# Performance work log

Measured on AMD Instinct MI355X. Metric: run time of the kernel, lower is better.

## Reference

```python
import jax, jax.numpy as jnp
import numpy as np

N_NODES = 50000


def graph_conv(h, src, dst, W, b, num_nodes):
    """GCN-style conv: transform node features, then sum messages over edges.
    h: [N, Din], W: [Din, Dout] -> out: [N, Dout].
    """
    m = (h @ W)[src]                                   # [E, Dout] per-edge messages
    agg = jax.ops.segment_sum(m, dst, num_segments=num_nodes)  # [N, Dout]
    return agg + b


def setup_inputs() -> dict:
    key = jax.random.key(0)
    ks = jax.random.split(key, 8)
    N, E, D = N_NODES, 800000, 128
    s = 1.0 / np.sqrt(2 * D)
    return {
        "node_feature": jax.random.normal(ks[0], (N, D), jnp.float32),
        "H_prev": jax.random.normal(ks[1], (N, D), jnp.float32),
        "edge_index": jax.random.randint(ks[2], (2, E), 0, N, jnp.int32),
        "W_main": jax.random.normal(ks[3], (D, D), jnp.float32) / np.sqrt(D),
        "b_main": jnp.zeros((D,), jnp.float32),
        "W_z": jax.random.normal(ks[4], (2 * D, D), jnp.float32) * s,
        "b_z": jnp.zeros((D,), jnp.float32),
        "W_r": jax.random.normal(ks[5], (2 * D, D), jnp.float32) * s,
        "b_r": jnp.zeros((D,), jnp.float32),
        "W_h": jax.random.normal(ks[6], (2 * D, D), jnp.float32) * s,
        "b_h": jnp.zeros((D,), jnp.float32),
    }


def reference(node_feature, H_prev, edge_index, W_main, b_main,
              W_z, b_z, W_r, b_r, W_h, b_h):
    N = node_feature.shape[0]
    src, dst = edge_index[0], edge_index[1]
    # main message-passing layer + post-layer activation (ReLU)
    X = jax.nn.relu(graph_conv(node_feature, src, dst, W_main, b_main, N))
    # GRU-gated graph convolutions
    cat_zr = jnp.concatenate([X, H_prev], axis=1)       # [N, 2D]
    Z = jax.nn.sigmoid(graph_conv(cat_zr, src, dst, W_z, b_z, N))
    R = jax.nn.sigmoid(graph_conv(cat_zr, src, dst, W_r, b_r, N))
    cat_h = jnp.concatenate([X, R * H_prev], axis=1)
    H_tilde = jnp.tanh(graph_conv(cat_h, src, dst, W_h, b_h, N))
    H_out = Z * H_prev + (1.0 - Z) * H_tilde
    return H_out
```

## Files before the change

### kernel.cpp

```cpp
#include <hip/hip_runtime.h>
#include <hip/hip_fp16.h>
#include <math.h>

typedef _Float16 f16;
typedef f16 f16x2 __attribute__((ext_vector_type(2)));
typedef f16 f16x4 __attribute__((ext_vector_type(4)));
typedef f16 f16x8 __attribute__((ext_vector_type(8)));
typedef float f32x4_t __attribute__((ext_vector_type(4)));

__device__ __forceinline__ float sigmoidf(float x) {
  return 1.0f / (1.0f + __expf(-x));
}

#define GLDS16(gp, lp)                                                     \
  __builtin_amdgcn_global_load_lds(                                        \
      (const __attribute__((address_space(1))) void*)(gp),                 \
      (__attribute__((address_space(3))) void*)(lp), 16, 0, 0)

__global__ void zero_ints(int* __restrict__ p, int n) {
  int i = blockIdx.x * blockDim.x + threadIdx.x;
  if (i < n) p[i] = 0;
}

__global__ void bucket_hist(const int* __restrict__ dst, int* __restrict__ bcntP,
                            int E, int NB) {
  __shared__ int h[256];
  for (int i = threadIdx.x; i < NB; i += 256) h[i] = 0;
  __syncthreads();
  int base = (blockIdx.x * 256 + threadIdx.x) * 4;
  if (base + 3 < E) {
    int4 d = *(const int4*)&dst[base];
    atomicAdd(&h[d.x >> 8], 1);
    atomicAdd(&h[d.y >> 8], 1);
    atomicAdd(&h[d.z >> 8], 1);
    atomicAdd(&h[d.w >> 8], 1);
  } else {
    for (int e = base; e < E; ++e) atomicAdd(&h[dst[e] >> 8], 1);
  }
  __syncthreads();
  for (int i = threadIdx.x; i < NB; i += 256)
    if (h[i]) atomicAdd(&bcntP[i * 16], h[i]);
}

__global__ __launch_bounds__(256) void bucket_scan(const int* __restrict__ bcntP,
                                                   int* __restrict__ bbases,
                                                   int* __restrict__ gcurP, int NB) {
  __shared__ int wsum[4];
  const int tid = threadIdx.x, lane = tid & 63, wid = tid >> 6;
  int v = (tid < NB) ? bcntP[tid * 16] : 0;
  int x = v;
  #pragma unroll
  for (int d = 1; d < 64; d <<= 1) { int y = __shfl_up(x, d); if (lane >= d) x += y; }
  if (lane == 63) wsum[wid] = x;
  __syncthreads();
  if (wid == 0 && lane < 4) {
    int ws = wsum[lane];
    #pragma unroll
    for (int d = 1; d < 4; d <<= 1) { int y = __shfl_up(ws, d); if (lane >= d) ws += y; }
    wsum[lane] = ws;
  }
  __syncthreads();
  int excl = x - v + (wid ? wsum[wid - 1] : 0);
  if (tid < NB) { bbases[tid] = excl; gcurP[tid * 16] = excl; }
  if (tid == NB - 1) bbases[NB] = excl + v;
}

__global__ __launch_bounds__(256) void partition_v2(const int* __restrict__ src,
                                                    const int* __restrict__ dst,
                                                    int* __restrict__ gcurP,
                                                    unsigned int* __restrict__ bin,
                                                    int E, int NB) {
  __shared__ int bhist[256];
  __shared__ int bofs[257];
  __shared__ int gbase[256];
  __shared__ unsigned int recs[4096];
  const int tid = threadIdx.x;
  const int base = blockIdx.x * 4096;
  bhist[tid] = 0;
  __syncthreads();
  unsigned int rec[16];
  int bk[16];
  #pragma unroll
  for (int k = 0; k < 16; ++k) {
    int e = base + tid + k * 256;
    if (e < E) {
      int d = dst[e];
      rec[k] = (unsigned int)(src[e] & 0xFFFF) | ((unsigned int)(d & 255) << 16);
      bk[k] = d >> 8;
      atomicAdd(&bhist[bk[k]], 1);
    } else {
      bk[k] = -1;
    }
  }
  __syncthreads();
  if (tid < 64) {
    int l = tid;
    int v0 = bhist[4 * l], v1 = bhist[4 * l + 1];
    int v2 = bhist[4 * l + 2], v3 = bhist[4 * l + 3];
    int s1 = v0 + v1, s2 = s1 + v2, t = s2 + v3;
    int x = t;
    #pragma unroll
    for (int d = 1; d < 64; d <<= 1) { int y = __shfl_up(x, d); if (l >= d) x += y; }
    int basex = x - t;
    bofs[4 * l] = basex;
    bofs[4 * l + 1] = basex + v0;
    bofs[4 * l + 2] = basex + s1;
    bofs[4 * l + 3] = basex + s2;
    if (l == 63) bofs[256] = x;
  }
  __syncthreads();
  if (tid < NB && bhist[tid] > 0)
    gbase[tid] = atomicAdd(&gcurP[tid * 16], bhist[tid]);
  bhist[tid] = bofs[tid];
  __syncthreads();
  #pragma unroll
  for (int k = 0; k < 16; ++k) {
    if (bk[k] >= 0) {
      int p = atomicAdd(&bhist[bk[k]], 1);
      recs[p] = rec[k];
    }
  }
  __syncthreads();
  const int total = bofs[256];
  for (int i = tid; i < total; i += 256) {
    int lo = 0, hi = 256;
    #pragma unroll
    for (int s = 0; s < 8; ++s) {
      int mid = (lo + hi) >> 1;
      if (bofs[mid] <= i) lo = mid; else hi = mid;
    }
    bin[gbase[lo] + (i - bofs[lo])] = recs[i];
  }
}

__global__ __launch_bounds__(256) void bucket_sort(const unsigned int* __restrict__ bin,
                                                   const int* __restrict__ bbases,
                                                   unsigned short* __restrict__ eidx,
                                                   int* __restrict__ off,
                                                   int N, int NB) {
  const int b = blockIdx.x;
  const int bb = bbases[b], be = bbases[b + 1];
  const int cntb = be - bb;
  const int d0 = b << 8;
  const int ndst = min(256, N - d0);
  __shared__ int hist[256];
  __shared__ int lofs[256];
  __shared__ int cnt2[256];
  __shared__ unsigned short srt[8192];
  const int tid = threadIdx.x;
  hist[tid] = 0;
  cnt2[tid] = 0;
  __syncthreads();
  for (int i = bb + tid; i < be; i += 256)
    atomicAdd(&hist[(bin[i] >> 16) & 255], 1);
  __syncthreads();
  if (tid < 64) {
    int l = tid;
    int v0 = hist[4 * l], v1 = hist[4 * l + 1], v2 = hist[4 * l + 2], v3 = hist[4 * l + 3];
    int s1 = v0 + v1, s2 = s1 + v2, t = s2 + v3;
    int x = t;
    #pragma unroll
    for (int d = 1; d < 64; d <<= 1) { int y = __shfl_up(x, d); if (l >= d) x += y; }
    int basex = x - t;
    lofs[4 * l] = basex;
    lofs[4 * l + 1] = basex + v0;
    lofs[4 * l + 2] = basex + s1;
    lofs[4 * l + 3] = basex + s2;
  }
  __syncthreads();
  if (tid < ndst) off[d0 + tid] = bb + lofs[tid];
  if (b == NB - 1 && tid == 0) off[N] = be;
  if (cntb <= 8192) {
    for (int i = bb + tid; i < be; i += 256) {
      unsigned int r = bin[i];
      int ld = (r >> 16) & 255;
      int p = lofs[ld] + atomicAdd(&cnt2[ld], 1);
      srt[p] = (unsigned short)(r & 0xFFFF);
    }
    __syncthreads();
    for (int i = tid; i < cntb; i += 256) eidx[bb + i] = srt[i];
  } else {
    for (int i = bb + tid; i < be; i += 256) {
      unsigned int r = bin[i];
      int ld = (r >> 16) & 255;
      int p = bb + lofs[ld] + atomicAdd(&cnt2[ld], 1);
      eidx[p] = (unsigned short)(r & 0xFFFF);
    }
  }
}

__global__ void count_kernel(const int* __restrict__ dst, int* __restrict__ cnt, int E) {
  int base = (blockIdx.x * blockDim.x + threadIdx.x) * 4;
  if (base + 3 < E) {
    int4 d = *(const int4*)&dst[base];
    atomicAdd(&cnt[d.x], 1);
    atomicAdd(&cnt[d.y], 1);
    atomicAdd(&cnt[d.z], 1);
    atomicAdd(&cnt[d.w], 1);
  } else {
    for (int e = base; e < E; ++e) atomicAdd(&cnt[dst[e]], 1);
  }
}

__global__ __launch_bounds__(1024) void scan_local(const int* __restrict__ cnt,
                                                   int* __restrict__ off,
                                                   int* __restrict__ psum, int n) {
  __shared__ int wsum[16];
  const int tid = threadIdx.x, lane = tid & 63, wid = tid >> 6;
  int i = blockIdx.x * 1024 + tid;
  int v = (i < n) ? cnt[i] : 0;
  int x = v;
  #pragma unroll
  for (int d = 1; d < 64; d <<= 1) { int y = __shfl_up(x, d); if (lane >= d) x += y; }
  if (lane == 63) wsum[wid] = x;
  __syncthreads();
  if (wid == 0) {
    int ws = (lane < 16) ? wsum[lane] : 0;
    #pragma unroll
    for (int d = 1; d < 16; d <<= 1) { int y = __shfl_up(ws, d); if (lane >= d) ws += y; }
    if (lane < 16) wsum[lane] = ws;
  }
  __syncthreads();
  int excl = x - v + (wid ? wsum[wid - 1] : 0);
  if (i < n) off[i] = excl;
  if (tid == 1023) psum[blockIdx.x] = wsum[15];
}

__global__ __launch_bounds__(1024) void scan_carry(int* __restrict__ psum,
                                                   int* __restrict__ off,
                                                   int* __restrict__ cur, int nb, int n) {
  __shared__ int wsum[16];
  const int tid = threadIdx.x, lane = tid & 63, wid = tid >> 6;
  int v = (tid < nb) ? psum[tid] : 0;
  int x = v;
  #pragma unroll
  for (int d = 1; d < 64; d <<= 1) { int y = __shfl_up(x, d); if (lane >= d) x += y; }
  if (lane == 63) wsum[wid] = x;
  __syncthreads();
  if (wid == 0) {
    int ws = (lane < 16) ? wsum[lane] : 0;
    #pragma unroll
    for (int d = 1; d < 16; d <<= 1) { int y = __shfl_up(ws, d); if (lane >= d) ws += y; }
    if (lane < 16) wsum[lane] = ws;
  }
  __syncthreads();
  int excl = x - v + (wid ? wsum[wid - 1] : 0);
  if (tid < nb) psum[tid] = excl;
  if (tid == 1023) { off[n] = wsum[15]; cur[n] = wsum[15]; }
}

__global__ __launch_bounds__(1024) void scan_add(int* __restrict__ off, int* __restrict__ cur,
                                                 const int* __restrict__ psum, int n) {
  int i = blockIdx.x * 1024 + threadIdx.x;
  if (i < n) {
    int t = off[i] + psum[blockIdx.x];
    off[i] = t;
    cur[i] = t;
  }
}

__global__ void fill_kernel(const int* __restrict__ src, const int* __restrict__ dst,
                            int* __restrict__ cur, int* __restrict__ eidx, int E) {
  int base = (blockIdx.x * blockDim.x + threadIdx.x) * 4;
  if (base + 3 < E) {
    int4 d = *(const int4*)&dst[base];
    int4 s = *(const int4*)&src[base];
    int p0 = atomicAdd(&cur[d.x], 1);
    int p1 = atomicAdd(&cur[d.y], 1);
    int p2 = atomicAdd(&cur[d.z], 1);
    int p3 = atomicAdd(&cur[d.w], 1);
    eidx[p0] = s.x; eidx[p1] = s.y; eidx[p2] = s.z; eidx[p3] = s.w;
  } else {
    for (int e = base; e < E; ++e) {
      int p = atomicAdd(&cur[dst[e]], 1);
      eidx[p] = src[e];
    }
  }
}

__global__ void pack_nfh(const float* __restrict__ nf, const float* __restrict__ H,
                         f16* __restrict__ P0, int N) {
  int gid = blockIdx.x * blockDim.x + threadIdx.x;
  int w = gid >> 6;
  if (w >= N) return;
  int lane = threadIdx.x & 63;
  const float* S = (lane < 32) ? nf : H;
  int c = (lane & 31) * 4;
  float4 u = *(const float4*)&S[(size_t)w * 128 + c];
  f16x4 o = {(f16)u.x, (f16)u.y, (f16)u.z, (f16)u.w};
  *(f16x4*)&P0[(size_t)w * 256 + (lane < 32 ? 0 : 128) + c] = o;
}

__global__ void wtrans_all(const float* __restrict__ Wm, const float* __restrict__ Wz,
                           const float* __restrict__ Wr, const float* __restrict__ Wh,
                           f16* __restrict__ WtM, f16* __restrict__ WtZR,
                           f16* __restrict__ WtH) {
  __shared__ float tile[32][33];
  const float* W;
  f16* O;
  int K;
  switch (blockIdx.z) {
    case 0: W = Wm; O = WtM; K = 128; break;
    case 1: W = Wz; O = WtZR; K = 256; break;
    case 2: W = Wr; O = WtZR + 128 * 256; K = 256; break;
    default: W = Wh; O = WtH; K = 256; break;
  }
  int bk = blockIdx.x * 32, bn = blockIdx.y * 32;
  if (bk >= K) return;
  int tx = threadIdx.x, ty = threadIdx.y;
  #pragma unroll
  for (int i = 0; i < 4; ++i)
    tile[ty + 8 * i][tx] = W[(size_t)(bk + ty + 8 * i) * 128 + bn + tx];
  __syncthreads();
  #pragma unroll
  for (int i = 0; i < 4; ++i)
    O[(size_t)(bn + ty + 8 * i) * K + bk + tx] = (f16)tile[tx][ty + 8 * i];
}

template <int COLS, typename IDX>
__global__ __launch_bounds__(256) void gather(const f16* __restrict__ P,
                                              const int* __restrict__ off,
                                              const IDX* __restrict__ eidx,
                                              f16* __restrict__ O, int N) {
  constexpr int NG = (COLS == 256) ? 2 : 4;
  constexpr int GL = 64 / NG;
  constexpr int SH = (COLS == 256) ? 9 : 8;
  int gid = blockIdx.x * blockDim.x + threadIdx.x;
  int wave = gid >> 6;
  int lane = threadIdx.x & 63;
  int g = lane / GL, lg = lane % GL;
  int node = wave * NG + g;
  if (node >= N) return;
  const int beg = off[node], end = off[node + 1];
  const char* base = (const char*)P + lg * 16;
  float a0 = 0.f, a1 = 0.f, a2 = 0.f, a3 = 0.f;
  float a4 = 0.f, a5 = 0.f, a6 = 0.f, a7 = 0.f;
  int j = beg;
  for (; j + 8 <= end; j += 8) {
    f16x8 v[8];
    #pragma unroll
    for (int u = 0; u < 8; ++u)
      v[u] = *(const f16x8*)(base + (((int)eidx[j + u]) << SH));
    #pragma unroll
    for (int u = 0; u < 8; ++u) {
      a0 += (float)v[u][0]; a1 += (float)v[u][1];
      a2 += (float)v[u][2]; a3 += (float)v[u][3];
      a4 += (float)v[u][4]; a5 += (float)v[u][5];
      a6 += (float)v[u][6]; a7 += (float)v[u][7];
    }
  }
  for (; j < end; ++j) {
    f16x8 v = *(const f16x8*)(base + (((int)eidx[j]) << SH));
    a0 += (float)v[0]; a1 += (float)v[1]; a2 += (float)v[2]; a3 += (float)v[3];
    a4 += (float)v[4]; a5 += (float)v[5]; a6 += (float)v[6]; a7 += (float)v[7];
  }
  f16x8 o = {(f16)a0, (f16)a1, (f16)a2, (f16)a3, (f16)a4, (f16)a5, (f16)a6, (f16)a7};
  *(f16x8*)&O[(size_t)node * COLS + lg * 8] = o;
}

template <int TERMS, int EPI>
__global__ __launch_bounds__(256) void gemm_mfma(
    const f16* __restrict__ A0, int lda0, const f16* __restrict__ A1, int lda1,
    const f16* __restrict__ Wt,
    const float* __restrict__ b0, const float* __restrict__ b1,
    const float* __restrict__ H, const f16* __restrict__ Zh,
    f16* __restrict__ O0, f16* __restrict__ O1, float* __restrict__ Ofp, int N) {
  constexpr int KTOT = TERMS * 128;
  constexpr int T = KTOT / 64;
  __shared__ __align__(16) f16 As[2][64][64];
  __shared__ __align__(16) f16 Bs[2][128][64];
  const int tid = threadIdx.x;
  const int l = tid & 63;
  const int wv = __builtin_amdgcn_readfirstlane(tid >> 6);
  const int fr = l & 15;
  const int q = l >> 4;
  const int brow = blockIdx.x * 64;
  const int coff = blockIdx.y * 128;
  const int rowA = wv * 16 + fr;
  const int sl8 = l >> 3, sg = l & 7;

  f32x4_t acc[8];
  #pragma unroll
  for (int n = 0; n < 8; ++n) acc[n] = (f32x4_t)0.0f;

  auto stage = [&](int t, int buf) {
    const bool sel1 = (TERMS == 2) && (t >= 2);
    const f16* __restrict__ A = sel1 ? A1 : A0;
    const int lda = sel1 ? lda1 : lda0;
    const int klocal = (t & 1) * 64;
    const int kk = t * 64;
    f16* Asf = &As[buf][0][0];
    f16* Bsf = &Bs[buf][0][0];
    #pragma unroll
    for (int c = 0; c < 2; ++c) {
      int chunk = wv + c * 4;
      int row = chunk * 8 + sl8;
      int gs = sg ^ (row & 7);
      int grow = brow + row;
      if (grow > N - 1) grow = N - 1;
      GLDS16(A + (size_t)grow * lda + klocal + gs * 8, Asf + chunk * 512);
    }
    #pragma unroll
    for (int c = 0; c < 4; ++c) {
      int chunk = wv + c * 4;
      int col = chunk * 8 + sl8;
      int gs = sg ^ (col & 7);
      GLDS16(Wt + (size_t)(coff + col) * KTOT + kk + gs * 8, Bsf + chunk * 512);
    }
  };

  stage(0, 0);
  #pragma unroll
  for (int t = 0; t < T; ++t) {
    if (t + 1 < T) {
      stage(t + 1, (t + 1) & 1);
      asm volatile("s_waitcnt vmcnt(6)" ::: "memory");
    } else {
      asm volatile("s_waitcnt vmcnt(0)" ::: "memory");
    }
    __builtin_amdgcn_s_barrier();
    const int buf = t & 1;
    #pragma unroll
    for (int ks = 0; ks < 2; ++ks) {
      f16x8 a = *(const f16x8*)&As[buf][rowA][((ks * 4 + q) ^ (rowA & 7)) * 8];
      f16x8 bfr[8];
      #pragma unroll
      for (int n = 0; n < 8; ++n) {
        int colB = n * 16 + fr;
        bfr[n] = *(const f16x8*)&Bs[buf][colB][((ks * 4 + q) ^ (colB & 7)) * 8];
      }
      #pragma unroll
      for (int n = 0; n < 8; ++n)
        acc[n] = __builtin_amdgcn_mfma_f32_16x16x32_f16(a, bfr[n], acc[n], 0, 0, 0);
    }
    asm volatile("s_waitcnt lgkmcnt(0)" ::: "memory");
    __builtin_amdgcn_s_barrier();
  }

  const int row0 = brow + wv * 16 + q * 4;
  #pragma unroll
  for (int n = 0; n < 8; ++n) {
    int colL = n * 16 + fr;
    if (EPI == 0) {
      float bias = b0[colL];
      #pragma unroll
      for (int r = 0; r < 4; ++r) {
        int row = row0 + r;
        if (row < N)
          O0[(size_t)row * 128 + colL] = (f16)fmaxf(acc[n][r] + bias, 0.f);
      }
    } else if (EPI == 1) {
      if (coff == 0) {
        float bias = b0[colL];
        #pragma unroll
        for (int r = 0; r < 4; ++r) {
          int row = row0 + r;
          if (row < N)
            O0[(size_t)row * 128 + colL] = (f16)sigmoidf(acc[n][r] + bias);
        }
      } else {
        float bias = b1[colL];
        #pragma unroll
        for (int r = 0; r < 4; ++r) {
          int row = row0 + r;
          if (row < N) {
            float g = sigmoidf(acc[n][r] + bias) * H[(size_t)row * 128 + colL];
            O1[(size_t)row * 128 + colL] = (f16)g;
          }
        }
      }
    } else {
      float bias = b0[colL];
      #pragma unroll
      for (int r = 0; r < 4; ++r) {
        int row = row0 + r;
        if (row < N) {
          size_t p = (size_t)row * 128 + colL;
          float ht = tanhf(acc[n][r] + bias);
          float z = (float)Zh[p];
          float h = H[p];
          Ofp[p] = z * h + (1.0f - z) * ht;
        }
      }
    }
  }
}


extern "C" void kernel_launch(void* const* d_in, const int* in_sizes, int n_in,
                              void* d_out, int out_size, void* d_ws, size_t ws_size,
                              hipStream_t stream) {
  const float* nf = (const float*)d_in[0];
  const float* H  = (const float*)d_in[1];
  const int*   ei = (const int*)d_in[2];
  const float* Wm = (const float*)d_in[3];
  const float* bm = (const float*)d_in[4];
  const float* Wz = (const float*)d_in[5];
  const float* bz = (const float*)d_in[6];
  const float* Wr = (const float*)d_in[7];
  const float* br = (const float*)d_in[8];
  const float* Wh = (const float*)d_in[9];
  const float* bh = (const float*)d_in[10];
  float* out = (float*)d_out;

  const int N = in_sizes[0] / 128;
  const int E = in_sizes[2] / 2;
  const int* src = ei;
  const int* dst = ei + E;

  char* ws = (char*)d_ws;
  size_t o = 0;
  auto alloc = [&](size_t bytes) {
    char* p = ws + o;
    o = (o + bytes + 511) & ~(size_t)511;
    return p;
  };
  const int NB = (N + 255) >> 8;
  const int nbch = (N + 1023) / 1024;
  int* bcntP  = (int*)alloc((size_t)NB * 16 * 4);
  int* gcurP  = (int*)alloc((size_t)NB * 16 * 4);
  int* bbases = (int*)alloc((size_t)(NB + 1) * 4);
  unsigned int* bin = (unsigned int*)alloc((size_t)E * 4);
  int* off    = (int*)alloc((size_t)(N + 1) * 4);
  int* cur    = (int*)alloc((size_t)(N + 1) * 4);
  int* cnt    = (int*)alloc((size_t)N * 4);
  int* psum   = (int*)alloc((size_t)nbch * 4);
  void* eidx  = (void*)alloc((size_t)E * 4);
  f16* WtM    = (f16*)alloc((size_t)128 * 128 * 2);
  f16* WtZR   = (f16*)alloc((size_t)256 * 256 * 2);
  f16* WtH    = (f16*)alloc((size_t)128 * 256 * 2);
  f16* P0     = (f16*)alloc((size_t)N * 256 * 2);
  f16* X      = (f16*)alloc((size_t)N * 128 * 2);
  f16* AX     = (f16*)alloc((size_t)N * 128 * 2);
  f16* G      = (f16*)alloc((size_t)N * 128 * 2);
  f16* AP0    = (f16*)d_out;
  f16* Zh     = X;
  f16* AG     = P0;

  const bool small = (N <= 65536);
  const int qblk = ((E + 3) / 4 + 255) / 256;

  if (small) {
    zero_ints<<<(NB * 16 + 255) / 256, 256, 0, stream>>>(bcntP, NB * 16);
    bucket_hist<<<qblk, 256, 0, stream>>>(dst, bcntP, E, NB);
    bucket_scan<<<1, 256, 0, stream>>>(bcntP, bbases, gcurP, NB);
    partition_v2<<<(E + 4095) / 4096, 256, 0, stream>>>(src, dst, gcurP, bin, E, NB);
    bucket_sort<<<NB, 256, 0, stream>>>(bin, bbases, (unsigned short*)eidx, off, N, NB);
  } else {
    zero_ints<<<(N + 255) / 256, 256, 0, stream>>>(cnt, N);
    count_kernel<<<qblk, 256, 0, stream>>>(dst, cnt, E);
    scan_local<<<nbch, 1024, 0, stream>>>(cnt, off, psum, N);
    scan_carry<<<1, 1024, 0, stream>>>(psum, off, cur, nbch, N);
    scan_add<<<nbch, 1024, 0, stream>>>(off, cur, psum, N);
    fill_kernel<<<qblk, 256, 0, stream>>>(src, dst, cur, (int*)eidx, E);
  }

  wtrans_all<<<dim3(8, 4, 4), dim3(32, 8), 0, stream>>>(Wm, Wz, Wr, Wh, WtM, WtZR, WtH);
  const int pblk = (N * 64 + 255) / 256;
  pack_nfh<<<pblk, 256, 0, stream>>>(nf, H, P0, N);

  const int mblk = (N + 63) / 64;
  const int g256 = (N + 7) / 8;
  const int g128 = (N + 15) / 16;

  if (small)
    gather<256, unsigned short><<<g256, 256, 0, stream>>>(P0, off, (const unsigned short*)eidx, AP0, N);
  else
    gather<256, int><<<g256, 256, 0, stream>>>(P0, off, (const int*)eidx, AP0, N);

  gemm_mfma<1, 0><<<dim3(mblk, 1), 256, 0, stream>>>(
      AP0, 256, nullptr, 0, WtM, bm, nullptr, nullptr, nullptr, X, nullptr, nullptr, N);

  if (small)
    gather<128, unsigned short><<<g128, 256, 0, stream>>>(X, off, (const unsigned short*)eidx, AX, N);
  else
    gather<128, int><<<g128, 256, 0, stream>>>(X, off, (const int*)eidx, AX, N);

  gemm_mfma<2, 1><<<dim3(mblk, 2), 256, 0, stream>>>(
      AX, 128, AP0 + 128, 256, WtZR, bz, br, H, nullptr, Zh, G, nullptr, N);

  if (small)
    gather<128, unsigned short><<<g128, 256, 0, stream>>>(G, off, (const unsigned short*)eidx, AG, N);
  else
    gather<128, int><<<g128, 256, 0, stream>>>(G, off, (const int*)eidx, AG, N);

  gemm_mfma<2, 2><<<dim3(mblk, 1), 256, 0, stream>>>(
      AX, 128, AG, 128, WtH, bh, nullptr, H, Zh, nullptr, nullptr, out, N);
}
```

Baseline: 281.8 us.

## Fuse neighbor aggregation into MFMA GEMM kernels, one launch per graph conv

Replaces the separate gather and GEMM kernels with one fused kernel per stage. Each block aggregates the neighbor features for its 64 destination rows straight into LDS, then runs the MFMA GEMM on them while double-buffering the weight tiles. This removes the global round-trips of the aggregated intermediates and three kernel launches. The Z and R GEMMs are also merged into a single 256-wide output pass, so their aggregation is done once. In exchange, the gather now runs with only 64 rows per block, which limits occupancy, and it adds extra LDS use and new workspace buffers.

```diff
diff --git a/kernel.cpp b/kernel.cpp
--- a/kernel.cpp
+++ b/kernel.cpp
@@ -3,7 +3,6 @@
 #include <math.h>
 
 typedef _Float16 f16;
-typedef f16 f16x2 __attribute__((ext_vector_type(2)));
 typedef f16 f16x4 __attribute__((ext_vector_type(4)));
 typedef f16 f16x8 __attribute__((ext_vector_type(8)));
 typedef float f32x4_t __attribute__((ext_vector_type(4)));
@@ -317,121 +316,137 @@
     O[(size_t)(bn + ty + 8 * i) * K + bk + tx] = (f16)tile[tx][ty + 8 * i];
 }
 
-template <int COLS, typename IDX>
-__global__ __launch_bounds__(256) void gather(const f16* __restrict__ P,
-                                              const int* __restrict__ off,
-                                              const IDX* __restrict__ eidx,
-                                              f16* __restrict__ O, int N) {
-  constexpr int NG = (COLS == 256) ? 2 : 4;
-  constexpr int GL = 64 / NG;
-  constexpr int SH = (COLS == 256) ? 9 : 8;
-  int gid = blockIdx.x * blockDim.x + threadIdx.x;
-  int wave = gid >> 6;
-  int lane = threadIdx.x & 63;
-  int g = lane / GL, lg = lane % GL;
-  int node = wave * NG + g;
-  if (node >= N) return;
-  const int beg = off[node], end = off[node + 1];
-  const char* base = (const char*)P + lg * 16;
-  float a0 = 0.f, a1 = 0.f, a2 = 0.f, a3 = 0.f;
-  float a4 = 0.f, a5 = 0.f, a6 = 0.f, a7 = 0.f;
-  int j = beg;
-  for (; j + 8 <= end; j += 8) {
-    f16x8 v[8];
-    #pragma unroll
-    for (int u = 0; u < 8; ++u)
-      v[u] = *(const f16x8*)(base + (((int)eidx[j + u]) << SH));
-    #pragma unroll
-    for (int u = 0; u < 8; ++u) {
-      a0 += (float)v[u][0]; a1 += (float)v[u][1];
-      a2 += (float)v[u][2]; a3 += (float)v[u][3];
-      a4 += (float)v[u][4]; a5 += (float)v[u][5];
-      a6 += (float)v[u][6]; a7 += (float)v[u][7];
-    }
-  }
-  for (; j < end; ++j) {
-    f16x8 v = *(const f16x8*)(base + (((int)eidx[j]) << SH));
-    a0 += (float)v[0]; a1 += (float)v[1]; a2 += (float)v[2]; a3 += (float)v[3];
-    a4 += (float)v[4]; a5 += (float)v[5]; a6 += (float)v[6]; a7 += (float)v[7];
-  }
-  f16x8 o = {(f16)a0, (f16)a1, (f16)a2, (f16)a3, (f16)a4, (f16)a5, (f16)a6, (f16)a7};
-  *(f16x8*)&O[(size_t)node * COLS + lg * 8] = o;
-}
-
-template <int TERMS, int EPI>
-__global__ __launch_bounds__(256) void gemm_mfma(
-    const f16* __restrict__ A0, int lda0, const f16* __restrict__ A1, int lda1,
+template <int V, typename IDX>
+__global__ __launch_bounds__(256) void fused_agg_gemm(
+    const f16* __restrict__ P, const f16* __restrict__ Dn,
+    const int* __restrict__ off, const IDX* __restrict__ eidx,
     const f16* __restrict__ Wt,
     const float* __restrict__ b0, const float* __restrict__ b1,
-    const float* __restrict__ H, const f16* __restrict__ Zh,
-    f16* __restrict__ O0, f16* __restrict__ O1, float* __restrict__ Ofp, int N) {
-  constexpr int KTOT = TERMS * 128;
-  constexpr int T = KTOT / 64;
-  __shared__ __align__(16) f16 As[2][64][64];
-  __shared__ __align__(16) f16 Bs[2][128][64];
+    const float* __restrict__ Hf, const f16* __restrict__ ZhIn,
+    f16* __restrict__ O0, f16* __restrict__ O1, f16* __restrict__ Oagg,
+    float* __restrict__ Ofp, int N) {
+  constexpr int KTOT  = (V == 1) ? 128 : 256;
+  constexpr int NOUT  = (V == 2) ? 256 : 128;
+  constexpr int AG    = KTOT / 8;
+  constexpr int CH    = KTOT / 32;
+  constexpr int NFRAG = NOUT / 16;
+  constexpr int IB    = NOUT / 64;
+  constexpr int GRPL  = (V == 1) ? 32 : 16;
+  constexpr int NGRP  = 256 / GRPL;
+  constexpr int ROUNDS = 64 / NGRP;
+  constexpr int SH    = (V == 1) ? 9 : 8;
+
+  __shared__ __align__(16) f16 Ald[64 * AG * 8];
+  __shared__ __align__(16) f16 Bld[2][NOUT * 4 * 8];
+
   const int tid = threadIdx.x;
   const int l = tid & 63;
   const int wv = __builtin_amdgcn_readfirstlane(tid >> 6);
-  const int fr = l & 15;
-  const int q = l >> 4;
+  const int fr = l & 15, q = l >> 4;
   const int brow = blockIdx.x * 64;
-  const int coff = blockIdx.y * 128;
+
+  auto aslot = [&](int g, int row) -> int {
+    if constexpr (V == 1) return g ^ (row & 15);
+    else return (g & 16) | ((g & 15) ^ (row & 15));
+  };
+
+  auto stageB = [&](int c, int buf) {
+    #pragma unroll
+    for (int i = 0; i < IB; ++i) {
+      int colbase = (wv * IB + i) * 16;
+      int col = colbase + (l >> 2);
+      int gs = (l & 3) ^ (col & 3);
+      GLDS16(Wt + (size_t)col * KTOT + c * 32 + gs * 8, &Bld[buf][colbase * 32]);
+    }
+  };
+
+  stageB(0, 0);
+
+  {
+    const int gi = (V == 1) ? (l >> 5) : (l >> 4);
+    const int lg = l & (GRPL - 1);
+    const int groupId = wv * (64 / GRPL) + gi;
+    const char* base = (const char*)P + lg * 16;
+    for (int r = 0; r < ROUNDS; ++r) {
+      int dstL = r * NGRP + groupId;
+      int dst = brow + dstL;
+      if (dst < N) {
+        int beg = off[dst], end = off[dst + 1];
+        float a0 = 0.f, a1 = 0.f, a2 = 0.f, a3 = 0.f;
+        float a4 = 0.f, a5 = 0.f, a6 = 0.f, a7 = 0.f;
+        int j = beg;
+        for (; j + 8 <= end; j += 8) {
+          f16x8 v[8];
+          #pragma unroll
+          for (int u = 0; u < 8; ++u)
+            v[u] = *(const f16x8*)(base + (((int)eidx[j + u]) << SH));
+          #pragma unroll
+          for (int u = 0; u < 8; ++u) {
+            a0 += (float)v[u][0]; a1 += (float)v[u][1];
+            a2 += (float)v[u][2]; a3 += (float)v[u][3];
+            a4 += (float)v[u][4]; a5 += (float)v[u][5];
+            a6 += (float)v[u][6]; a7 += (float)v[u][7];
+          }
+        }
+        for (; j < end; ++j) {
+          f16x8 v = *(const f16x8*)(base + (((int)eidx[j]) << SH));
+          a0 += (float)v[0]; a1 += (float)v[1]; a2 += (float)v[2]; a3 += (float)v[3];
+          a4 += (float)v[4]; a5 += (float)v[5]; a6 += (float)v[6]; a7 += (float)v[7];
+        }
+        f16x8 o = {(f16)a0, (f16)a1, (f16)a2, (f16)a3,
+                   (f16)a4, (f16)a5, (f16)a6, (f16)a7};
+        if constexpr (V == 1) {
+          if (lg < 16)
+            *(f16x8*)&Ald[(dstL * AG + aslot(lg, dstL)) * 8] = o;
+          else
+            *(f16x8*)&O1[(size_t)dst * 128 + (lg - 16) * 8] = o;
+        } else if constexpr (V == 2) {
+          *(f16x8*)&Ald[(dstL * AG + aslot(lg, dstL)) * 8] = o;
+          *(f16x8*)&Oagg[(size_t)dst * 128 + lg * 8] = o;
+        } else {
+          *(f16x8*)&Ald[(dstL * AG + aslot(16 + lg, dstL)) * 8] = o;
+        }
+      }
+    }
+  }
+
+  if constexpr (V != 1) {
+    #pragma unroll
+    for (int i = 0; i < 4; ++i) {
+      int gidx = i * 256 + tid;
+      int row = gidx >> 4, gk = gidx & 15;
+      int gr = brow + row;
+      if (gr > N - 1) gr = N - 1;
+      f16x8 v = *(const f16x8*)&Dn[(size_t)gr * 128 + gk * 8];
+      int g = (V == 2) ? (16 + gk) : gk;
+      *(f16x8*)&Ald[(row * AG + aslot(g, row)) * 8] = v;
+    }
+  }
+
+  asm volatile("s_waitcnt vmcnt(0) lgkmcnt(0)" ::: "memory");
+  __builtin_amdgcn_s_barrier();
+
+  f32x4_t acc[NFRAG];
+  #pragma unroll
+  for (int n = 0; n < NFRAG; ++n) acc[n] = (f32x4_t)0.0f;
   const int rowA = wv * 16 + fr;
-  const int sl8 = l >> 3, sg = l & 7;
-
-  f32x4_t acc[8];
-  #pragma unroll
-  for (int n = 0; n < 8; ++n) acc[n] = (f32x4_t)0.0f;
-
-  auto stage = [&](int t, int buf) {
-    const bool sel1 = (TERMS == 2) && (t >= 2);
-    const f16* __restrict__ A = sel1 ? A1 : A0;
-    const int lda = sel1 ? lda1 : lda0;
-    const int klocal = (t & 1) * 64;
-    const int kk = t * 64;
-    f16* Asf = &As[buf][0][0];
-    f16* Bsf = &Bs[buf][0][0];
-    #pragma unroll
-    for (int c = 0; c < 2; ++c) {
-      int chunk = wv + c * 4;
-      int row = chunk * 8 + sl8;
-      int gs = sg ^ (row & 7);
-      int grow = brow + row;
-      if (grow > N - 1) grow = N - 1;
-      GLDS16(A + (size_t)grow * lda + klocal + gs * 8, Asf + chunk * 512);
-    }
-    #pragma unroll
-    for (int c = 0; c < 4; ++c) {
-      int chunk = wv + c * 4;
-      int col = chunk * 8 + sl8;
-      int gs = sg ^ (col & 7);
-      GLDS16(Wt + (size_t)(coff + col) * KTOT + kk + gs * 8, Bsf + chunk * 512);
-    }
-  };
-
-  stage(0, 0);
-  #pragma unroll
-  for (int t = 0; t < T; ++t) {
-    if (t + 1 < T) {
-      stage(t + 1, (t + 1) & 1);
-      asm volatile("s_waitcnt vmcnt(6)" ::: "memory");
+
+  #pragma unroll
+  for (int c = 0; c < CH; ++c) {
+    if (c + 1 < CH) {
+      stageB(c + 1, (c + 1) & 1);
+      asm volatile("s_waitcnt vmcnt(%0)" :: "i"(IB) : "memory");
     } else {
       asm volatile("s_waitcnt vmcnt(0)" ::: "memory");
     }
     __builtin_amdgcn_s_barrier();
-    const int buf = t & 1;
-    #pragma unroll
-    for (int ks = 0; ks < 2; ++ks) {
-      f16x8 a = *(const f16x8*)&As[buf][rowA][((ks * 4 + q) ^ (rowA & 7)) * 8];
-      f16x8 bfr[8];
-      #pragma unroll
-      for (int n = 0; n < 8; ++n) {
-        int colB = n * 16 + fr;
-        bfr[n] = *(const f16x8*)&Bs[buf][colB][((ks * 4 + q) ^ (colB & 7)) * 8];
-      }
-      #pragma unroll
-      for (int n = 0; n < 8; ++n)
-        acc[n] = __builtin_amdgcn_mfma_f32_16x16x32_f16(a, bfr[n], acc[n], 0, 0, 0);
+    const int buf = c & 1;
+    f16x8 a = *(const f16x8*)&Ald[(rowA * AG + aslot(c * 4 + q, rowA)) * 8];
+    #pragma unroll
+    for (int n = 0; n < NFRAG; ++n) {
+      int colB = n * 16 + fr;
+      f16x8 b = *(const f16x8*)&Bld[buf][(colB * 4 + (q ^ (colB & 3))) * 8];
+      acc[n] = __builtin_amdgcn_mfma_f32_16x16x32_f16(a, b, acc[n], 0, 0, 0);
     }
     asm volatile("s_waitcnt lgkmcnt(0)" ::: "memory");
     __builtin_amdgcn_s_barrier();
@@ -439,46 +454,47 @@
 
   const int row0 = brow + wv * 16 + q * 4;
   #pragma unroll
-  for (int n = 0; n < 8; ++n) {
-    int colL = n * 16 + fr;
-    if (EPI == 0) {
-      float bias = b0[colL];
+  for (int n = 0; n < NFRAG; ++n) {
+    int colB = n * 16 + fr;
+    if constexpr (V == 1) {
+      float bias = b0[colB];
       #pragma unroll
       for (int r = 0; r < 4; ++r) {
         int row = row0 + r;
         if (row < N)
-          O0[(size_t)row * 128 + colL] = (f16)fmaxf(acc[n][r] + bias, 0.f);
+          O0[(size_t)row * 128 + colB] = (f16)fmaxf(acc[n][r] + bias, 0.f);
       }
-    } else if (EPI == 1) {
-      if (coff == 0) {
-        float bias = b0[colL];
+    } else if constexpr (V == 2) {
+      if (n < 8) {
+        float bias = b0[colB];
         #pragma unroll
         for (int r = 0; r < 4; ++r) {
           int row = row0 + r;
           if (row < N)
-            O0[(size_t)row * 128 + colL] = (f16)sigmoidf(acc[n][r] + bias);
+            O0[(size_t)row * 128 + colB] = (f16)sigmoidf(acc[n][r] + bias);
         }
       } else {
+        int colL = colB - 128;
         float bias = b1[colL];
         #pragma unroll
         for (int r = 0; r < 4; ++r) {
           int row = row0 + r;
           if (row < N) {
-            float g = sigmoidf(acc[n][r] + bias) * H[(size_t)row * 128 + colL];
+            float g = sigmoidf(acc[n][r] + bias) * Hf[(size_t)row * 128 + colL];
             O1[(size_t)row * 128 + colL] = (f16)g;
           }
         }
       }
     } else {
-      float bias = b0[colL];
+      float bias = b0[colB];
       #pragma unroll
       for (int r = 0; r < 4; ++r) {
         int row = row0 + r;
         if (row < N) {
-          size_t p = (size_t)row * 128 + colL;
+          size_t p = (size_t)row * 128 + colB;
           float ht = tanhf(acc[n][r] + bias);
-          float z = (float)Zh[p];
-          float h = H[p];
+          float z = (float)ZhIn[p];
+          float h = Hf[p];
           Ofp[p] = z * h + (1.0f - z) * ht;
         }
       }
@@ -531,11 +547,10 @@
   f16* WtH    = (f16*)alloc((size_t)128 * 256 * 2);
   f16* P0     = (f16*)alloc((size_t)N * 256 * 2);
   f16* X      = (f16*)alloc((size_t)N * 128 * 2);
+  f16* AH     = (f16*)alloc((size_t)N * 128 * 2);
   f16* AX     = (f16*)alloc((size_t)N * 128 * 2);
   f16* G      = (f16*)alloc((size_t)N * 128 * 2);
-  f16* AP0    = (f16*)d_out;
-  f16* Zh     = X;
-  f16* AG     = P0;
+  f16* Zh     = (f16*)alloc((size_t)N * 128 * 2);
 
   const bool small = (N <= 65536);
   const int qblk = ((E + 3) / 4 + 255) / 256;
@@ -560,30 +575,28 @@
   pack_nfh<<<pblk, 256, 0, stream>>>(nf, H, P0, N);
 
   const int mblk = (N + 63) / 64;
-  const int g256 = (N + 7) / 8;
-  const int g128 = (N + 15) / 16;
-
-  if (small)
-    gather<256, unsigned short><<<g256, 256, 0, stream>>>(P0, off, (const unsigned short*)eidx, AP0, N);
-  else
-    gather<256, int><<<g256, 256, 0, stream>>>(P0, off, (const int*)eidx, AP0, N);
-
-  gemm_mfma<1, 0><<<dim3(mblk, 1), 256, 0, stream>>>(
-      AP0, 256, nullptr, 0, WtM, bm, nullptr, nullptr, nullptr, X, nullptr, nullptr, N);
-
-  if (small)
-    gather<128, unsigned short><<<g128, 256, 0, stream>>>(X, off, (const unsigned short*)eidx, AX, N);
-  else
-    gather<128, int><<<g128, 256, 0, stream>>>(X, off, (const int*)eidx, AX, N);
-
-  gemm_mfma<2, 1><<<dim3(mblk, 2), 256, 0, stream>>>(
-      AX, 128, AP0 + 128, 256, WtZR, bz, br, H, nullptr, Zh, G, nullptr, N);
-
-  if (small)
-    gather<128, unsigned short><<<g128, 256, 0, stream>>>(G, off, (const unsigned short*)eidx, AG, N);
-  else
-    gather<128, int><<<g128, 256, 0, stream>>>(G, off, (const int*)eidx, AG, N);
-
-  gemm_mfma<2, 2><<<dim3(mblk, 1), 256, 0, stream>>>(
-      AX, 128, AG, 128, WtH, bh, nullptr, H, Zh, nullptr, nullptr, out, N);
-}
+
+  if (small) {
+    using IDX = unsigned short;
+    fused_agg_gemm<1, IDX><<<mblk, 256, 0, stream>>>(
+        P0, nullptr, off, (const IDX*)eidx, WtM, bm, nullptr, nullptr, nullptr,
+        X, AH, nullptr, nullptr, N);
+    fused_agg_gemm<2, IDX><<<mblk, 256, 0, stream>>>(
+        X, AH, off, (const IDX*)eidx, WtZR, bz, br, H, nullptr,
+        Zh, G, AX, nullptr, N);
+    fused_agg_gemm<3, IDX><<<mblk, 256, 0, stream>>>(
+        G, AX, off, (const IDX*)eidx, WtH, bh, nullptr, H, Zh,
+        nullptr, nullptr, nullptr, out, N);
+  } else {
+    using IDX = int;
+    fused_agg_gemm<1, IDX><<<mblk, 256, 0, stream>>>(
+        P0, nullptr, off, (const IDX*)eidx, WtM, bm, nullptr, nullptr, nullptr,
+        X, AH, nullptr, nullptr, N);
+    fused_agg_gemm<2, IDX><<<mblk, 256, 0, stream>>>(
+        X, AH, off, (const IDX*)eidx, WtZR, bz, br, H, nullptr,
+        Zh, G, AX, nullptr, N);
+    fused_agg_gemm<3, IDX><<<mblk, 256, 0, stream>>>(
+        G, AX, off, (const IDX*)eidx, WtH, bh, nullptr, H, Zh,
+        nullptr, nullptr, nullptr, out, N);
+  }
+}
```

Result: slower. 351.3 us (+24.7%).
